# Kernel tuning notes

Hardware: AMD Instinct MI355X
Metric: run time of the kernel (lower is better)

The kernel has to match this reference:

```python
import jax, jax.numpy as jnp
import numpy as np

V, H, B, S = 32000, 512, 128, 64

def setup_inputs() -> dict:
    key = jax.random.key(0)
    ks = jax.random.split(key, 16)
    sc = 0.02
    return {
        "input_ids": jax.random.randint(ks[0], (B,), 0, V),
        "h0": jax.random.normal(ks[1], (1, B, H), jnp.float32),
        "c0": jax.random.normal(ks[2], (1, B, H), jnp.float32),
        "encoder_outputs": jax.random.normal(ks[3], (B, S, H), jnp.float32),
        "emb": jax.random.normal(ks[4], (V, H), jnp.float32) * sc,
        "attn_W": jax.random.normal(ks[5], (H, 2 * H), jnp.float32) * sc,
        "attn_b": jnp.zeros((H,), jnp.float32),
        "v": jax.random.uniform(ks[6], (H,), jnp.float32),
        "W_ih": jax.random.normal(ks[7], (4 * H, 2 * H), jnp.float32) * sc,
        "W_hh": jax.random.normal(ks[8], (4 * H, H), jnp.float32) * sc,
        "b_ih": jnp.zeros((4 * H,), jnp.float32),
        "b_hh": jnp.zeros((4 * H,), jnp.float32),
        "fc_W": jax.random.normal(ks[9], (V, H), jnp.float32) * sc,
        "fc_b": jnp.zeros((V,), jnp.float32),
    }

def reference(input_ids, h0, c0, encoder_outputs, emb, attn_W, attn_b, v,
              W_ih, W_hh, b_ih, b_hh, fc_W, fc_b):
    # Embedding lookup: [B, H]
    embedded = emb[input_ids]
    h = h0[0]  # top-layer hidden state [B, H]
    c = c0[0]
    # Bahdanau attention over encoder outputs [B, S, H]
    h_rep = jnp.broadcast_to(h[:, None, :], encoder_outputs.shape)
    cat = jnp.concatenate([h_rep, encoder_outputs], axis=-1)  # [B, S, 2H]
    energy = jnp.tanh(jnp.einsum('bsd,hd->bsh', cat, attn_W) + attn_b)
    scores = jnp.einsum('bsh,h->bs', energy, v)
    attn_weights = jax.nn.softmax(scores, axis=1)  # [B, S]
    context = jnp.einsum('bs,bsh->bh', attn_weights, encoder_outputs)
    # Single LSTM cell step (PyTorch gate order i, f, g, o)
    rnn_in = jnp.concatenate([embedded, context], axis=-1)  # [B, 2H]
    gates = rnn_in @ W_ih.T + b_ih + h @ W_hh.T + b_hh  # [B, 4H]
    i, f, g, o = jnp.split(gates, 4, axis=-1)
    c_new = jax.nn.sigmoid(f) * c + jax.nn.sigmoid(i) * jnp.tanh(g)
    h_new = jax.nn.sigmoid(o) * jnp.tanh(c_new)
    prediction = h_new @ fc_W.T + fc_b  # [B, V]
    return prediction, h_new[None], c_new[None]
```

## Files before the change

kernel.cpp:

```cpp
#include <hip/hip_runtime.h>

typedef __bf16 bf16;
typedef __bf16 bf16x8 __attribute__((ext_vector_type(8)));
typedef float f32x4 __attribute__((ext_vector_type(4)));

#define VOCAB 32000
#define HID 512
#define BATCH 128
#define SEQ 64

__device__ inline bf16x8 cvt8(float4 a, float4 b) {
  bf16x8 r;
  r[0] = (bf16)a.x; r[1] = (bf16)a.y; r[2] = (bf16)a.z; r[3] = (bf16)a.w;
  r[4] = (bf16)b.x; r[5] = (bf16)b.y; r[6] = (bf16)b.z; r[7] = (bf16)b.w;
  return r;
}

__device__ inline float fast_tanh(float x) {
  x = fminf(fmaxf(x, -15.f), 15.f);
  float e = __expf(2.f * x);
  return (e - 1.f) / (e + 1.f);
}
__device__ inline float fast_sig(float x) {
  return 1.f / (1.f + __expf(-x));
}

__global__ __launch_bounds__(512) void k_prep(
    const float* __restrict__ h0, const float* __restrict__ attn_W,
    const float* __restrict__ attn_b, bf16* __restrict__ W2p,
    float* __restrict__ e1) {
  int b = blockIdx.x, tid = threadIdx.x;
  __shared__ float h0s[512];
  h0s[tid] = h0[b * 512 + tid];
  __syncthreads();
  int h = tid;
  const float* wrow = attn_W + (size_t)h * 1024;
  float acc = attn_b[h];
#pragma unroll 4
  for (int d = 0; d < 512; d += 4) {
    float4 wv = *(const float4*)(wrow + d);
    float4 hv = *(const float4*)(&h0s[d]);
    acc += hv.x * wv.x + hv.y * wv.y + hv.z * wv.z + hv.w * wv.w;
  }
  e1[b * 512 + h] = acc;

  int gid = b * 512 + tid;
  if (gid < 512 * 64) {
    int hh = gid >> 6, kc8 = gid & 63;
    const float* src = attn_W + (size_t)hh * 1024 + 512 + kc8 * 8;
    bf16x8 v = cvt8(((const float4*)src)[0], ((const float4*)src)[1]);
    int kchunk = kc8 >> 2, klane = kc8 & 3;
    int ntile = hh >> 4, nlane = hh & 15;
    int lane = klane * 16 + nlane;
    *(bf16x8*)(W2p + ((size_t)(kchunk * 32 + ntile) * 64 + lane) * 8) = v;
  }
}

__global__ __launch_bounds__(512) void k_attn(
    const float* __restrict__ enc, const bf16* __restrict__ W2p,
    const float* __restrict__ e1, const float* __restrict__ vvec,
    const float* __restrict__ emb, const int* __restrict__ ids,
    const float* __restrict__ h0, bf16* __restrict__ Acat,
    float* __restrict__ gates_ws) {
  __shared__ char smem[65536];
  bf16* encA = (bf16*)smem;
  float* spart = (float*)smem;
  float* wgt = (float*)(smem + 2048);
  float* ctxp = (float*)(smem + 2304);

  int b = blockIdx.x, tid = threadIdx.x;
  int w = tid >> 6, lane = tid & 63;
  int l15 = lane & 15, lq = lane >> 4;
  const float* encb = enc + (size_t)b * SEQ * HID;

  {
    int gid = b * 512 + tid;
    float4 z = {0.f, 0.f, 0.f, 0.f};
    ((float4*)gates_ws)[gid] = z;
  }

#pragma unroll
  for (int i = 0; i < 8; ++i) {
    int cl = tid + i * 512;
    int row = cl >> 6;
    int c = cl & 63;
    int phys = c ^ (row & 7);
    const float4* src = (const float4*)(encb + row * 512 + c * 8);
    bf16x8 v = cvt8(src[0], src[1]);
    *(bf16x8*)(encA + row * 512 + phys * 8) = v;
  }
  __syncthreads();

  f32x4 acc[4][4];
#pragma unroll
  for (int mt = 0; mt < 4; ++mt)
#pragma unroll
    for (int jn = 0; jn < 4; ++jn) acc[mt][jn] = (f32x4)0.f;

  for (int kc = 0; kc < 16; ++kc) {
    bf16x8 bfr[4], af[4];
#pragma unroll
    for (int jn = 0; jn < 4; ++jn) {
      int nt = w * 4 + jn;
      bfr[jn] = *(const bf16x8*)(W2p + ((size_t)(kc * 32 + nt) * 64 + lane) * 8);
    }
#pragma unroll
    for (int mt = 0; mt < 4; ++mt) {
      int row = mt * 16 + l15;
      int c = kc * 4 + lq;
      int phys = c ^ (row & 7);
      af[mt] = *(const bf16x8*)(encA + row * 512 + phys * 8);
    }
#pragma unroll
    for (int mt = 0; mt < 4; ++mt)
#pragma unroll
      for (int jn = 0; jn < 4; ++jn)
        acc[mt][jn] = __builtin_amdgcn_mfma_f32_16x16x32_bf16(
            af[mt], bfr[jn], acc[mt][jn], 0, 0, 0);
  }
  __syncthreads();

  float p[4][4];
#pragma unroll
  for (int mt = 0; mt < 4; ++mt)
#pragma unroll
    for (int r = 0; r < 4; ++r) p[mt][r] = 0.f;
#pragma unroll
  for (int jn = 0; jn < 4; ++jn) {
    int h = (w * 4 + jn) * 16 + l15;
    float e1v = e1[b * 512 + h];
    float vv = vvec[h];
#pragma unroll
    for (int mt = 0; mt < 4; ++mt)
#pragma unroll
      for (int r = 0; r < 4; ++r)
        p[mt][r] += vv * fast_tanh(acc[mt][jn][r] + e1v);
  }
#pragma unroll
  for (int mt = 0; mt < 4; ++mt)
#pragma unroll
    for (int r = 0; r < 4; ++r) {
      float x = p[mt][r];
      x += __shfl_xor(x, 1);
      x += __shfl_xor(x, 2);
      x += __shfl_xor(x, 4);
      x += __shfl_xor(x, 8);
      p[mt][r] = x;
    }
  if (l15 == 0) {
#pragma unroll
    for (int mt = 0; mt < 4; ++mt)
#pragma unroll
      for (int r = 0; r < 4; ++r) {
        int s = mt * 16 + lq * 4 + r;
        spart[w * 64 + s] = p[mt][r];
      }
  }
  __syncthreads();

  if (tid < 64) {
    float sc = 0.f;
#pragma unroll
    for (int ww = 0; ww < 8; ++ww) sc += spart[ww * 64 + tid];
    float mx = sc;
    for (int m = 32; m; m >>= 1) mx = fmaxf(mx, __shfl_xor(mx, m));
    float e = __expf(sc - mx);
    float sm = e;
    for (int m = 32; m; m >>= 1) sm += __shfl_xor(sm, m);
    wgt[tid] = e / sm;
  }
  __syncthreads();

  {
    int hc = tid & 63, sg = tid >> 6;
    float a8[8];
#pragma unroll
    for (int j = 0; j < 8; ++j) a8[j] = 0.f;
    for (int s = sg * 8; s < sg * 8 + 8; ++s) {
      float wv = wgt[s];
      const float4* src = (const float4*)(encb + s * 512 + hc * 8);
      float4 x0 = src[0], x1 = src[1];
      a8[0] += wv * x0.x; a8[1] += wv * x0.y; a8[2] += wv * x0.z; a8[3] += wv * x0.w;
      a8[4] += wv * x1.x; a8[5] += wv * x1.y; a8[6] += wv * x1.z; a8[7] += wv * x1.w;
    }
#pragma unroll
    for (int j = 0; j < 8; ++j) ctxp[sg * 512 + hc * 8 + j] = a8[j];
  }
  __syncthreads();

  {
    int h = tid;
    float c = 0.f;
#pragma unroll
    for (int g = 0; g < 8; ++g) c += ctxp[g * 512 + h];
    int id = ids[b];
    Acat[(size_t)b * 1536 + h] = (bf16)emb[(size_t)id * 512 + h];
    Acat[(size_t)b * 1536 + 512 + h] = (bf16)c;
    Acat[(size_t)b * 1536 + 1024 + h] = (bf16)h0[b * 512 + h];
  }
}

__global__ __launch_bounds__(512) void k_gates(
    const bf16* __restrict__ Acat, const float* __restrict__ W_ih,
    const float* __restrict__ W_hh, float* __restrict__ gates_ws) {
  int nb = blockIdx.x, ks = blockIdx.y;
  __shared__ bf16 Wl[128 * 40];
  int tid = threadIdx.x, w = tid >> 6, lane = tid & 63;
  int l15 = lane & 15, lq = lane >> 4;
  int wrow = w & 3, wcol = w >> 2;
  f32x4 acc[2][4];
#pragma unroll
  for (int i = 0; i < 2; ++i)
#pragma unroll
    for (int j = 0; j < 4; ++j) acc[i][j] = (f32x4)0.f;

  for (int kt = 0; kt < 8; ++kt) {
    int kb = ks * 256 + kt * 32;
    {
      int r = tid >> 2, sub = tid & 3;
      int grow = nb * 128 + r;
      const float* src = (kb < 1024)
                             ? (W_ih + (size_t)grow * 1024 + kb + sub * 8)
                             : (W_hh + (size_t)grow * 512 + (kb - 1024) + sub * 8);
      bf16x8 v = cvt8(((const float4*)src)[0], ((const float4*)src)[1]);
      *(bf16x8*)(Wl + r * 40 + sub * 8) = v;
    }
    __syncthreads();
    bf16x8 af[2], bfr[4];
#pragma unroll
    for (int mi = 0; mi < 2; ++mi) {
      int m = (wrow * 2 + mi) * 16 + l15;
      af[mi] = *(const bf16x8*)(Acat + (size_t)m * 1536 + kb + lq * 8);
    }
#pragma unroll
    for (int jn = 0; jn < 4; ++jn) {
      int nt = wcol * 4 + jn;
      bfr[jn] = *(const bf16x8*)(Wl + (nt * 16 + l15) * 40 + lq * 8);
    }
#pragma unroll
    for (int mi = 0; mi < 2; ++mi)
#pragma unroll
      for (int jn = 0; jn < 4; ++jn)
        acc[mi][jn] = __builtin_amdgcn_mfma_f32_16x16x32_bf16(
            af[mi], bfr[jn], acc[mi][jn], 0, 0, 0);
    __syncthreads();
  }
#pragma unroll
  for (int mi = 0; mi < 2; ++mi)
#pragma unroll
    for (int jn = 0; jn < 4; ++jn)
#pragma unroll
      for (int r = 0; r < 4; ++r) {
        int bb = (wrow * 2 + mi) * 16 + lq * 4 + r;
        int n = nb * 128 + wcol * 64 + jn * 16 + l15;
        atomicAdd(&gates_ws[(size_t)bb * 2048 + n], acc[mi][jn][r]);
      }
}

__global__ __launch_bounds__(512) void k_cell(
    const float* __restrict__ gates_ws, const float* __restrict__ b_ih,
    const float* __restrict__ b_hh, const float* __restrict__ c0,
    float* __restrict__ out, bf16* __restrict__ hnewb) {
  int idx = blockIdx.x * 512 + threadIdx.x;
  int b = idx >> 9, h = idx & 511;
  const float* g = gates_ws + (size_t)b * 2048;
  float iv = g[h] + b_ih[h] + b_hh[h];
  float fv = g[512 + h] + b_ih[512 + h] + b_hh[512 + h];
  float gv = g[1024 + h] + b_ih[1024 + h] + b_hh[1024 + h];
  float ov = g[1536 + h] + b_ih[1536 + h] + b_hh[1536 + h];
  float cn = fast_sig(fv) * c0[idx] + fast_sig(iv) * fast_tanh(gv);
  float hn = fast_sig(ov) * fast_tanh(cn);
  out[4096000 + idx] = hn;
  out[4096000 + 65536 + idx] = cn;
  hnewb[idx] = (bf16)hn;
}

__global__ __launch_bounds__(512) void k_fc(
    const bf16* __restrict__ hnewb, const float* __restrict__ fc_W,
    const float* __restrict__ fc_b, float* __restrict__ out) {
  int nb = blockIdx.x;
  int vb = nb * 128;
  __shared__ bf16 Wl[128 * 40];
  int tid = threadIdx.x, w = tid >> 6, lane = tid & 63;
  int l15 = lane & 15, lq = lane >> 4;
  int wrow = w & 3, wcol = w >> 2;
  f32x4 acc[2][4];
#pragma unroll
  for (int i = 0; i < 2; ++i)
#pragma unroll
    for (int j = 0; j < 4; ++j) acc[i][j] = (f32x4)0.f;

  for (int kt = 0; kt < 16; ++kt) {
    int kb = kt * 32;
    {
      int r = tid >> 2, sub = tid & 3;
      const float* src = fc_W + (size_t)(vb + r) * 512 + kb + sub * 8;
      bf16x8 v = cvt8(((const float4*)src)[0], ((const float4*)src)[1]);
      *(bf16x8*)(Wl + r * 40 + sub * 8) = v;
    }
    __syncthreads();
    bf16x8 af[2], bfr[4];
#pragma unroll
    for (int mi = 0; mi < 2; ++mi) {
      int m = (wrow * 2 + mi) * 16 + l15;
      af[mi] = *(const bf16x8*)(hnewb + (size_t)m * 512 + kb + lq * 8);
    }
#pragma unroll
    for (int jn = 0; jn < 4; ++jn) {
      int nt = wcol * 4 + jn;
      bfr[jn] = *(const bf16x8*)(Wl + (nt * 16 + l15) * 40 + lq * 8);
    }
#pragma unroll
    for (int mi = 0; mi < 2; ++mi)
#pragma unroll
      for (int jn = 0; jn < 4; ++jn)
        acc[mi][jn] = __builtin_amdgcn_mfma_f32_16x16x32_bf16(
            af[mi], bfr[jn], acc[mi][jn], 0, 0, 0);
    __syncthreads();
  }
#pragma unroll
  for (int mi = 0; mi < 2; ++mi)
#pragma unroll
    for (int jn = 0; jn < 4; ++jn) {
      int vv = vb + wcol * 64 + jn * 16 + l15;
      float bias = fc_b[vv];
#pragma unroll
      for (int r = 0; r < 4; ++r) {
        int bb = (wrow * 2 + mi) * 16 + lq * 4 + r;
        out[(size_t)bb * 32000 + vv] = acc[mi][jn][r] + bias;
      }
    }
}

extern "C" void kernel_launch(void* const* d_in, const int* in_sizes, int n_in,
                              void* d_out, int out_size, void* d_ws,
                              size_t ws_size, hipStream_t stream) {
  const int* ids = (const int*)d_in[0];
  const float* h0 = (const float*)d_in[1];
  const float* c0 = (const float*)d_in[2];
  const float* enc = (const float*)d_in[3];
  const float* emb = (const float*)d_in[4];
  const float* attn_W = (const float*)d_in[5];
  const float* attn_b = (const float*)d_in[6];
  const float* vvec = (const float*)d_in[7];
  const float* W_ih = (const float*)d_in[8];
  const float* W_hh = (const float*)d_in[9];
  const float* b_ih = (const float*)d_in[10];
  const float* b_hh = (const float*)d_in[11];
  const float* fc_W = (const float*)d_in[12];
  const float* fc_b = (const float*)d_in[13];
  float* out = (float*)d_out;
  char* ws = (char*)d_ws;

  bf16* W2p = (bf16*)ws;
  float* e1 = (float*)(ws + 524288);
  bf16* Acat = (bf16*)(ws + 786432);
  bf16* hnewb = (bf16*)(ws + 1179648);
  float* gates = (float*)(ws + 1310720);

  k_prep<<<128, 512, 0, stream>>>(h0, attn_W, attn_b, W2p, e1);
  k_attn<<<128, 512, 0, stream>>>(enc, W2p, e1, vvec, emb, ids, h0, Acat, gates);
  k_gates<<<dim3(16, 6), 512, 0, stream>>>(Acat, W_ih, W_hh, gates);
  k_cell<<<128, 512, 0, stream>>>(gates, b_ih, b_hh, c0, out, hnewb);
  k_fc<<<250, 512, 0, stream>>>(hnewb, fc_W, fc_b, out);
}
```

Baseline: 253.5 us.

## Fold h0 attention projection into MFMA loop and halve GEMM tile widths with prefetch

The prep kernel's scalar e1 = h0·W1 dot product is removed. The whole attn_W is packed to bf16 and e1 is now computed inside k_attn with MFMA, using the broadcast h0 row as the A operand. k_gates and k_fc shrink their N tile from 128 to 64, doubling the grid so more CUs are busy. They also register-prefetch the next fp32 weight slice before the MFMAs to overlap global loads with compute. The trade-offs are e1 at bf16 precision, redundant MFMA rows in the e1 step, and more atomics and blocks overall.

```diff
diff --git a/kernel.cpp b/kernel.cpp
--- a/kernel.cpp
+++ b/kernel.cpp
@@ -2,6 +2,7 @@
 
 typedef __bf16 bf16;
 typedef __bf16 bf16x8 __attribute__((ext_vector_type(8)));
+typedef __bf16 bf16x4 __attribute__((ext_vector_type(4)));
 typedef float f32x4 __attribute__((ext_vector_type(4)));
 
 #define VOCAB 32000
@@ -15,6 +16,11 @@
   r[4] = (bf16)b.x; r[5] = (bf16)b.y; r[6] = (bf16)b.z; r[7] = (bf16)b.w;
   return r;
 }
+__device__ inline bf16x4 cvt4(float4 a) {
+  bf16x4 r;
+  r[0] = (bf16)a.x; r[1] = (bf16)a.y; r[2] = (bf16)a.z; r[3] = (bf16)a.w;
+  return r;
+}
 
 __device__ inline float fast_tanh(float x) {
   x = fminf(fmaxf(x, -15.f), 15.f);
@@ -25,44 +31,27 @@
   return 1.f / (1.f + __expf(-x));
 }
 
-__global__ __launch_bounds__(512) void k_prep(
-    const float* __restrict__ h0, const float* __restrict__ attn_W,
-    const float* __restrict__ attn_b, bf16* __restrict__ W2p,
-    float* __restrict__ e1) {
-  int b = blockIdx.x, tid = threadIdx.x;
-  __shared__ float h0s[512];
-  h0s[tid] = h0[b * 512 + tid];
-  __syncthreads();
-  int h = tid;
-  const float* wrow = attn_W + (size_t)h * 1024;
-  float acc = attn_b[h];
-#pragma unroll 4
-  for (int d = 0; d < 512; d += 4) {
-    float4 wv = *(const float4*)(wrow + d);
-    float4 hv = *(const float4*)(&h0s[d]);
-    acc += hv.x * wv.x + hv.y * wv.y + hv.z * wv.z + hv.w * wv.w;
-  }
-  e1[b * 512 + h] = acc;
-
-  int gid = b * 512 + tid;
-  if (gid < 512 * 64) {
-    int hh = gid >> 6, kc8 = gid & 63;
-    const float* src = attn_W + (size_t)hh * 1024 + 512 + kc8 * 8;
-    bf16x8 v = cvt8(((const float4*)src)[0], ((const float4*)src)[1]);
-    int kchunk = kc8 >> 2, klane = kc8 & 3;
-    int ntile = hh >> 4, nlane = hh & 15;
-    int lane = klane * 16 + nlane;
-    *(bf16x8*)(W2p + ((size_t)(kchunk * 32 + ntile) * 64 + lane) * 8) = v;
-  }
+__global__ __launch_bounds__(512) void k_pack(
+    const float* __restrict__ attn_W, bf16* __restrict__ Wp) {
+  int gid = blockIdx.x * 512 + threadIdx.x;
+  int hh = gid >> 7;
+  int kc8 = gid & 127;
+  const float* src = attn_W + (size_t)hh * 1024 + kc8 * 8;
+  bf16x8 v = cvt8(((const float4*)src)[0], ((const float4*)src)[1]);
+  int kchunk = kc8 >> 2, klane = kc8 & 3;
+  int ntile = hh >> 4, nlane = hh & 15;
+  int lane = klane * 16 + nlane;
+  *(bf16x8*)(Wp + ((size_t)(kchunk * 32 + ntile) * 64 + lane) * 8) = v;
 }
 
 __global__ __launch_bounds__(512) void k_attn(
-    const float* __restrict__ enc, const bf16* __restrict__ W2p,
-    const float* __restrict__ e1, const float* __restrict__ vvec,
+    const float* __restrict__ enc, const bf16* __restrict__ Wp,
+    const float* __restrict__ attn_b, const float* __restrict__ vvec,
     const float* __restrict__ emb, const int* __restrict__ ids,
     const float* __restrict__ h0, bf16* __restrict__ Acat,
     float* __restrict__ gates_ws) {
   __shared__ char smem[65536];
+  __shared__ bf16 h0s[512];
   bf16* encA = (bf16*)smem;
   float* spart = (float*)smem;
   float* wgt = (float*)(smem + 2048);
@@ -78,6 +67,8 @@
     float4 z = {0.f, 0.f, 0.f, 0.f};
     ((float4*)gates_ws)[gid] = z;
   }
+
+  h0s[tid] = (bf16)h0[b * 512 + tid];
 
 #pragma unroll
   for (int i = 0; i < 8; ++i) {
@@ -92,22 +83,37 @@
   __syncthreads();
 
   f32x4 acc[4][4];
+  f32x4 acc_e1[4];
 #pragma unroll
   for (int mt = 0; mt < 4; ++mt)
 #pragma unroll
     for (int jn = 0; jn < 4; ++jn) acc[mt][jn] = (f32x4)0.f;
-
+#pragma unroll
+  for (int jn = 0; jn < 4; ++jn) acc_e1[jn] = (f32x4)0.f;
+
+#pragma unroll 4
   for (int kc = 0; kc < 16; ++kc) {
-    bf16x8 bfr[4], af[4];
+    bf16x8 af = *(const bf16x8*)(h0s + kc * 32 + lq * 8);
 #pragma unroll
     for (int jn = 0; jn < 4; ++jn) {
       int nt = w * 4 + jn;
-      bfr[jn] = *(const bf16x8*)(W2p + ((size_t)(kc * 32 + nt) * 64 + lane) * 8);
+      bf16x8 bfr = *(const bf16x8*)(Wp + ((size_t)(kc * 32 + nt) * 64 + lane) * 8);
+      acc_e1[jn] = __builtin_amdgcn_mfma_f32_16x16x32_bf16(af, bfr, acc_e1[jn], 0, 0, 0);
+    }
+  }
+
+#pragma unroll 2
+  for (int kc = 16; kc < 32; ++kc) {
+    bf16x8 bfr[4], af[4];
+#pragma unroll
+    for (int jn = 0; jn < 4; ++jn) {
+      int nt = w * 4 + jn;
+      bfr[jn] = *(const bf16x8*)(Wp + ((size_t)(kc * 32 + nt) * 64 + lane) * 8);
     }
 #pragma unroll
     for (int mt = 0; mt < 4; ++mt) {
       int row = mt * 16 + l15;
-      int c = kc * 4 + lq;
+      int c = (kc - 16) * 4 + lq;
       int phys = c ^ (row & 7);
       af[mt] = *(const bf16x8*)(encA + row * 512 + phys * 8);
     }
@@ -128,13 +134,13 @@
 #pragma unroll
   for (int jn = 0; jn < 4; ++jn) {
     int h = (w * 4 + jn) * 16 + l15;
-    float e1v = e1[b * 512 + h];
+    float bias = attn_b[h];
     float vv = vvec[h];
 #pragma unroll
     for (int mt = 0; mt < 4; ++mt)
 #pragma unroll
       for (int r = 0; r < 4; ++r)
-        p[mt][r] += vv * fast_tanh(acc[mt][jn][r] + e1v);
+        p[mt][r] += vv * fast_tanh(acc[mt][jn][r] + acc_e1[jn][r] + bias);
   }
 #pragma unroll
   for (int mt = 0; mt < 4; ++mt)
@@ -204,43 +210,48 @@
     const bf16* __restrict__ Acat, const float* __restrict__ W_ih,
     const float* __restrict__ W_hh, float* __restrict__ gates_ws) {
   int nb = blockIdx.x, ks = blockIdx.y;
-  __shared__ bf16 Wl[128 * 40];
+  __shared__ bf16 Wl[64 * 40];
   int tid = threadIdx.x, w = tid >> 6, lane = tid & 63;
   int l15 = lane & 15, lq = lane >> 4;
   int wrow = w & 3, wcol = w >> 2;
-  f32x4 acc[2][4];
+  int r = tid >> 3, sub = tid & 7;
+  int grow = nb * 64 + r;
+
+  f32x4 acc[2][2];
 #pragma unroll
   for (int i = 0; i < 2; ++i)
 #pragma unroll
-    for (int j = 0; j < 4; ++j) acc[i][j] = (f32x4)0.f;
-
+    for (int j = 0; j < 2; ++j) acc[i][j] = (f32x4)0.f;
+
+  auto load_tile = [&](int kt) -> float4 {
+    int kb = ks * 256 + kt * 32;
+    const float* src = (kb < 1024)
+                           ? (W_ih + (size_t)grow * 1024 + kb + sub * 4)
+                           : (W_hh + (size_t)grow * 512 + (kb - 1024) + sub * 4);
+    return *(const float4*)src;
+  };
+
+  float4 pf = load_tile(0);
   for (int kt = 0; kt < 8; ++kt) {
-    int kb = ks * 256 + kt * 32;
-    {
-      int r = tid >> 2, sub = tid & 3;
-      int grow = nb * 128 + r;
-      const float* src = (kb < 1024)
-                             ? (W_ih + (size_t)grow * 1024 + kb + sub * 8)
-                             : (W_hh + (size_t)grow * 512 + (kb - 1024) + sub * 8);
-      bf16x8 v = cvt8(((const float4*)src)[0], ((const float4*)src)[1]);
-      *(bf16x8*)(Wl + r * 40 + sub * 8) = v;
-    }
+    *(bf16x4*)(Wl + r * 40 + sub * 4) = cvt4(pf);
     __syncthreads();
-    bf16x8 af[2], bfr[4];
+    if (kt + 1 < 8) pf = load_tile(kt + 1);
+    int kglob = ks * 256 + kt * 32;
+    bf16x8 af[2], bfr[2];
 #pragma unroll
     for (int mi = 0; mi < 2; ++mi) {
       int m = (wrow * 2 + mi) * 16 + l15;
-      af[mi] = *(const bf16x8*)(Acat + (size_t)m * 1536 + kb + lq * 8);
-    }
-#pragma unroll
-    for (int jn = 0; jn < 4; ++jn) {
-      int nt = wcol * 4 + jn;
+      af[mi] = *(const bf16x8*)(Acat + (size_t)m * 1536 + kglob + lq * 8);
+    }
+#pragma unroll
+    for (int jn = 0; jn < 2; ++jn) {
+      int nt = wcol * 2 + jn;
       bfr[jn] = *(const bf16x8*)(Wl + (nt * 16 + l15) * 40 + lq * 8);
     }
 #pragma unroll
     for (int mi = 0; mi < 2; ++mi)
 #pragma unroll
-      for (int jn = 0; jn < 4; ++jn)
+      for (int jn = 0; jn < 2; ++jn)
         acc[mi][jn] = __builtin_amdgcn_mfma_f32_16x16x32_bf16(
             af[mi], bfr[jn], acc[mi][jn], 0, 0, 0);
     __syncthreads();
@@ -248,12 +259,12 @@
 #pragma unroll
   for (int mi = 0; mi < 2; ++mi)
 #pragma unroll
-    for (int jn = 0; jn < 4; ++jn)
-#pragma unroll
-      for (int r = 0; r < 4; ++r) {
-        int bb = (wrow * 2 + mi) * 16 + lq * 4 + r;
-        int n = nb * 128 + wcol * 64 + jn * 16 + l15;
-        atomicAdd(&gates_ws[(size_t)bb * 2048 + n], acc[mi][jn][r]);
+    for (int jn = 0; jn < 2; ++jn)
+#pragma unroll
+      for (int rr = 0; rr < 4; ++rr) {
+        int bb = (wrow * 2 + mi) * 16 + lq * 4 + rr;
+        int n = nb * 64 + (wcol * 2 + jn) * 16 + l15;
+        atomicAdd(&gates_ws[(size_t)bb * 2048 + n], acc[mi][jn][rr]);
       }
 }
 
@@ -278,42 +289,41 @@
 __global__ __launch_bounds__(512) void k_fc(
     const bf16* __restrict__ hnewb, const float* __restrict__ fc_W,
     const float* __restrict__ fc_b, float* __restrict__ out) {
-  int nb = blockIdx.x;
-  int vb = nb * 128;
-  __shared__ bf16 Wl[128 * 40];
+  int vb = blockIdx.x * 64;
+  __shared__ bf16 Wl[64 * 40];
   int tid = threadIdx.x, w = tid >> 6, lane = tid & 63;
   int l15 = lane & 15, lq = lane >> 4;
   int wrow = w & 3, wcol = w >> 2;
-  f32x4 acc[2][4];
+  int r = tid >> 3, sub = tid & 7;
+
+  f32x4 acc[2][2];
 #pragma unroll
   for (int i = 0; i < 2; ++i)
 #pragma unroll
-    for (int j = 0; j < 4; ++j) acc[i][j] = (f32x4)0.f;
-
+    for (int j = 0; j < 2; ++j) acc[i][j] = (f32x4)0.f;
+
+  const float* wbase = fc_W + (size_t)(vb + r) * 512 + sub * 4;
+  float4 pf = *(const float4*)(wbase);
   for (int kt = 0; kt < 16; ++kt) {
+    *(bf16x4*)(Wl + r * 40 + sub * 4) = cvt4(pf);
+    __syncthreads();
+    if (kt + 1 < 16) pf = *(const float4*)(wbase + (kt + 1) * 32);
     int kb = kt * 32;
-    {
-      int r = tid >> 2, sub = tid & 3;
-      const float* src = fc_W + (size_t)(vb + r) * 512 + kb + sub * 8;
-      bf16x8 v = cvt8(((const float4*)src)[0], ((const float4*)src)[1]);
-      *(bf16x8*)(Wl + r * 40 + sub * 8) = v;
-    }
-    __syncthreads();
-    bf16x8 af[2], bfr[4];
+    bf16x8 af[2], bfr[2];
 #pragma unroll
     for (int mi = 0; mi < 2; ++mi) {
       int m = (wrow * 2 + mi) * 16 + l15;
       af[mi] = *(const bf16x8*)(hnewb + (size_t)m * 512 + kb + lq * 8);
     }
 #pragma unroll
-    for (int jn = 0; jn < 4; ++jn) {
-      int nt = wcol * 4 + jn;
+    for (int jn = 0; jn < 2; ++jn) {
+      int nt = wcol * 2 + jn;
       bfr[jn] = *(const bf16x8*)(Wl + (nt * 16 + l15) * 40 + lq * 8);
     }
 #pragma unroll
     for (int mi = 0; mi < 2; ++mi)
 #pragma unroll
-      for (int jn = 0; jn < 4; ++jn)
+      for (int jn = 0; jn < 2; ++jn)
         acc[mi][jn] = __builtin_amdgcn_mfma_f32_16x16x32_bf16(
             af[mi], bfr[jn], acc[mi][jn], 0, 0, 0);
     __syncthreads();
@@ -321,13 +331,13 @@
 #pragma unroll
   for (int mi = 0; mi < 2; ++mi)
 #pragma unroll
-    for (int jn = 0; jn < 4; ++jn) {
-      int vv = vb + wcol * 64 + jn * 16 + l15;
+    for (int jn = 0; jn < 2; ++jn) {
+      int vv = vb + (wcol * 2 + jn) * 16 + l15;
       float bias = fc_b[vv];
 #pragma unroll
-      for (int r = 0; r < 4; ++r) {
-        int bb = (wrow * 2 + mi) * 16 + lq * 4 + r;
-        out[(size_t)bb * 32000 + vv] = acc[mi][jn][r] + bias;
+      for (int rr = 0; rr < 4; ++rr) {
+        int bb = (wrow * 2 + mi) * 16 + lq * 4 + rr;
+        out[(size_t)bb * 32000 + vv] = acc[mi][jn][rr] + bias;
       }
     }
 }
@@ -352,15 +362,14 @@
   float* out = (float*)d_out;
   char* ws = (char*)d_ws;
 
-  bf16* W2p = (bf16*)ws;
-  float* e1 = (float*)(ws + 524288);
-  bf16* Acat = (bf16*)(ws + 786432);
-  bf16* hnewb = (bf16*)(ws + 1179648);
-  float* gates = (float*)(ws + 1310720);
-
-  k_prep<<<128, 512, 0, stream>>>(h0, attn_W, attn_b, W2p, e1);
-  k_attn<<<128, 512, 0, stream>>>(enc, W2p, e1, vvec, emb, ids, h0, Acat, gates);
-  k_gates<<<dim3(16, 6), 512, 0, stream>>>(Acat, W_ih, W_hh, gates);
+  bf16* Wp = (bf16*)ws;
+  bf16* Acat = (bf16*)(ws + 1048576);
+  bf16* hnewb = (bf16*)(ws + 1441792);
+  float* gates = (float*)(ws + 1572864);
+
+  k_pack<<<128, 512, 0, stream>>>(attn_W, Wp);
+  k_attn<<<128, 512, 0, stream>>>(enc, Wp, attn_b, vvec, emb, ids, h0, Acat, gates);
+  k_gates<<<dim3(32, 6), 512, 0, stream>>>(Acat, W_ih, W_hh, gates);
   k_cell<<<128, 512, 0, stream>>>(gates, b_ih, b_hh, c0, out, hnewb);
-  k_fc<<<250, 512, 0, stream>>>(hnewb, fc_W, fc_b, out);
-}
+  k_fc<<<500, 512, 0, stream>>>(hnewb, fc_W, fc_b, out);
+}
```

Result: faster. 226.5 us (-10.7%).
